# Kernel optimization log

Measured on AMD Instinct MI355X. Metric: run time of the kernel, lower is better.

## Reference

```python
import jax, jax.numpy as jnp
import numpy as np

N = 768
C = 256  # in_features == out_features (required by Linear(in_features+3, 1))

def _leaky(x):
    return jnp.where(x >= 0, x, 0.2 * x)

def setup_inputs() -> dict:
    key = jax.random.key(0)
    ks = jax.random.split(key, 10)
    features = jax.random.normal(ks[0], (N, C), dtype=jnp.float32)
    coordinates = jax.random.normal(ks[1], (N, 3), dtype=jnp.float32)
    adj = jax.random.uniform(ks[2], (N, N), dtype=jnp.float32)  # unused by forward, kept for signature fidelity
    # Learned params
    FC = jax.random.normal(ks[3], (C, C), dtype=jnp.float32) * (1.414 / jnp.sqrt(C))
    # Conv1d(2,1,kernel=1): weight [out=1, in=2, k=1] -> 2 scalars + bias
    fc_w = jax.random.normal(ks[4], (2,), dtype=jnp.float32) * 0.5
    fc_b = jax.random.normal(ks[5], (1,), dtype=jnp.float32) * 0.1
    sc_w = jax.random.normal(ks[6], (2,), dtype=jnp.float32) * 0.5
    sc_b = jax.random.normal(ks[7], (1,), dtype=jnp.float32) * 0.1
    # Linear(C+3, 1)
    lin_w = jax.random.normal(ks[8], (C + 3,), dtype=jnp.float32) * (1.0 / jnp.sqrt(C + 3))
    lin_b = jax.random.normal(ks[9], (1,), dtype=jnp.float32) * 0.1
    return {"features": features, "coordinates": coordinates, "adj": adj,
            "FC": FC, "fc_w": fc_w, "fc_b": fc_b, "sc_w": sc_w, "sc_b": sc_b,
            "lin_w": lin_w, "lin_b": lin_b}

def reference(features, coordinates, adj, FC, fc_w, fc_b, sc_w, sc_b, lin_w, lin_b):
    n = features.shape[0]
    f_input = features @ FC  # [N, C]
    # torch's repeat(1,N).view + repeat(N,1) builds pairs (i, j); the 1x1 Conv1d over
    # the 2 stacked channels is exactly w0*x_i + w1*x_j + b, then LeakyReLU(0.2).
    f_map = _leaky(fc_w[0] * f_input[:, None, :] + fc_w[1] * f_input[None, :, :] + fc_b[0])  # [N,N,C]
    s_map = _leaky(sc_w[0] * coordinates[:, None, :] + sc_w[1] * coordinates[None, :, :] + sc_b[0])  # [N,N,3]
    # Linear(C+3, 1) on cat([f_map, s_map], -1), then LeakyReLU -> [N, N]
    scores = _leaky(jnp.einsum('ijc,c->ij', f_map, lin_w[:f_input.shape[1]])
                    + jnp.einsum('ijk,k->ij', s_map, lin_w[f_input.shape[1]:])
                    + lin_b[0])
    attention = jax.nn.softmax(scores, axis=1)  # row softmax (dim=1)
    h_prime = attention @ f_input  # [N, C]
    return jax.nn.elu(h_prime)  # concat=True path
```

## Files before the change

kernel.cpp:

```cpp
#include <hip/hip_runtime.h>
#include <math.h>

#define NN 768
#define CC 256
#define TI 3
#define JC 256
#define NJC 3

__device__ __forceinline__ float leaky(float x) { return x >= 0.0f ? x : 0.2f * x; }

__device__ __forceinline__ float waveMax(float v) {
    #pragma unroll
    for (int o = 32; o > 0; o >>= 1) v = fmaxf(v, __shfl_xor(v, o, 64));
    return v;
}
__device__ __forceinline__ float waveSum(float v) {
    #pragma unroll
    for (int o = 32; o > 0; o >>= 1) v += __shfl_xor(v, o, 64);
    return v;
}

__global__ __launch_bounds__(768) void k_prep(
    const float* __restrict__ features,
    const float* __restrict__ FC,
    const float* __restrict__ fc_w,
    const float* __restrict__ fc_b,
    const float* __restrict__ lin_w,
    float* __restrict__ f,
    float* __restrict__ g,
    float* __restrict__ D0,
    float* __restrict__ D1,
    float4* __restrict__ ut4)
{
    __shared__ float sA[TI * CC];
    __shared__ float sF[TI * CC];
    __shared__ float sredD[12], sredW[12];

    const int t  = threadIdx.x;
    const int r  = t >> 8;
    const int c  = t & 255;
    const int i0 = blockIdx.x * TI;

    sA[r * CC + c] = features[(i0 + r) * CC + c];
    __syncthreads();

    float a = 0.f;
    const float* fcp = FC + c;
    const float* ap  = sA + r * CC;
    #pragma unroll 8
    for (int k = 0; k < CC; ++k)
        a = fmaf(ap[k], fcp[k * CC], a);

    const float w1 = fc_w[1], b = fc_b[0];
    f[(i0 + r) * CC + c] = a;
    g[c * NN + i0 + r]   = fmaf(w1, a, b);
    sF[r * CC + c] = a;

    const float lw = lin_w[c];
    float dv = waveSum(lw * a);
    float wv = waveSum(lw);
    const int wid = t >> 6;
    if ((t & 63) == 0) { sredD[wid] = dv; sredW[wid] = wv; }
    __syncthreads();
    if (t < TI) {
        float D = sredD[t*4] + sredD[t*4+1] + sredD[t*4+2] + sredD[t*4+3];
        float W = sredW[t*4] + sredW[t*4+1] + sredW[t*4+2] + sredW[t*4+3];
        D0[i0 + t] = fc_w[0] * D;
        D1[i0 + t] = fmaf(w1, D, b * W);
    }
    if (t < CC) {
        const float w0 = fc_w[0];
        ut4[blockIdx.x * CC + t] = make_float4(w0 * sF[t],
                                               w0 * sF[CC + t],
                                               w0 * sF[2*CC + t],
                                               0.4f * lin_w[t]);
    }
}

__global__ __launch_bounds__(256) void k_attn(
    const float* __restrict__ f,
    const float* __restrict__ g,
    const float4* __restrict__ ut4,
    const float* __restrict__ D0,
    const float* __restrict__ D1,
    const float* __restrict__ coords,
    const float* __restrict__ sc_w,
    const float* __restrict__ sc_b,
    const float* __restrict__ lin_w,
    const float* __restrict__ lin_b,
    float* __restrict__ hp,
    float* __restrict__ Mp,
    float* __restrict__ Lp)
{
    __shared__ float4 su4[CC];
    __shared__ float  spart[4][TI][JC];
    __shared__ float4 pp[JC];
    __shared__ float  hpart[4][TI][CC];
    __shared__ float4 sredm4[4];
    __shared__ float4 sreds4[4];

    const int t    = threadIdx.x;
    const int it   = blockIdx.x & 255;
    const int jc   = blockIdx.x >> 8;
    const int i0   = it * TI;
    const int jb   = jc * JC;
    const int j    = jb + t;
    const int w    = t >> 6;
    const int lane = t & 63;

    su4[t] = ut4[(size_t)it * CC + t];
    __syncthreads();

    float4 a0 = make_float4(0.f,0.f,0.f,0.f);
    float4 a1 = a0, a2 = a0;
    const float4* gq = (const float4*)g + (size_t)(w << 6) * (NN/4) + (jb >> 2) + lane;
    const float4* su = su4 + (w << 6);
    #pragma unroll 8
    for (int cc = 0; cc < 64; ++cc) {
        float4 gv = gq[cc * (NN/4)];
        float4 u  = su[cc];
        a0.x = fmaf(u.w, fabsf(u.x + gv.x), a0.x);
        a0.y = fmaf(u.w, fabsf(u.x + gv.y), a0.y);
        a0.z = fmaf(u.w, fabsf(u.x + gv.z), a0.z);
        a0.w = fmaf(u.w, fabsf(u.x + gv.w), a0.w);
        a1.x = fmaf(u.w, fabsf(u.y + gv.x), a1.x);
        a1.y = fmaf(u.w, fabsf(u.y + gv.y), a1.y);
        a1.z = fmaf(u.w, fabsf(u.y + gv.z), a1.z);
        a1.w = fmaf(u.w, fabsf(u.y + gv.w), a1.w);
        a2.x = fmaf(u.w, fabsf(u.z + gv.x), a2.x);
        a2.y = fmaf(u.w, fabsf(u.z + gv.y), a2.y);
        a2.z = fmaf(u.w, fabsf(u.z + gv.z), a2.z);
        a2.w = fmaf(u.w, fabsf(u.z + gv.w), a2.w);
    }
    *(float4*)&spart[w][0][4*lane] = a0;
    *(float4*)&spart[w][1][4*lane] = a1;
    *(float4*)&spart[w][2][4*lane] = a2;
    __syncthreads();

    float accs[3];
    #pragma unroll
    for (int rr = 0; rr < TI; ++rr)
        accs[rr] = spart[0][rr][t] + spart[1][rr][t]
                 + spart[2][rr][t] + spart[3][rr][t];

    const float sw0 = sc_w[0], sw1 = sc_w[1], sb = sc_b[0], lb = lin_b[0];
    const float lw30 = lin_w[CC], lw31 = lin_w[CC+1], lw32 = lin_w[CC+2];
    const float cj0 = fmaf(sw1, coords[j*3+0], sb);
    const float cj1 = fmaf(sw1, coords[j*3+1], sb);
    const float cj2 = fmaf(sw1, coords[j*3+2], sb);
    const float d1  = D1[j];
    float scv[3];
    #pragma unroll
    for (int rr = 0; rr < TI; ++rr) {
        const int i = i0 + rr;
        float sd = lw30 * leaky(fmaf(sw0, coords[i*3+0], cj0))
                 + lw31 * leaky(fmaf(sw0, coords[i*3+1], cj1))
                 + lw32 * leaky(fmaf(sw0, coords[i*3+2], cj2));
        scv[rr] = leaky(accs[rr] + sd + 0.6f * (D0[i] + d1) + lb);
    }

    {
        float v0 = waveMax(scv[0]);
        float v1 = waveMax(scv[1]);
        float v2 = waveMax(scv[2]);
        if (lane == 0) sredm4[w] = make_float4(v0, v1, v2, 0.f);
    }
    __syncthreads();
    float m[TI];
    {
        float4 x0 = sredm4[0], x1 = sredm4[1], x2 = sredm4[2], x3 = sredm4[3];
        m[0] = fmaxf(fmaxf(x0.x, x1.x), fmaxf(x2.x, x3.x));
        m[1] = fmaxf(fmaxf(x0.y, x1.y), fmaxf(x2.y, x3.y));
        m[2] = fmaxf(fmaxf(x0.z, x1.z), fmaxf(x2.z, x3.z));
    }
    float e0 = __expf(scv[0] - m[0]);
    float e1 = __expf(scv[1] - m[1]);
    float e2 = __expf(scv[2] - m[2]);
    pp[t] = make_float4(e0, e1, e2, 0.f);
    {
        float v0 = waveSum(e0);
        float v1 = waveSum(e1);
        float v2 = waveSum(e2);
        if (lane == 0) sreds4[w] = make_float4(v0, v1, v2, 0.f);
    }
    __syncthreads();
    if (t < TI) {
        float4 s0 = sreds4[0], s1 = sreds4[1], s2 = sreds4[2], s3 = sreds4[3];
        float l = (t == 0) ? (s0.x + s1.x + s2.x + s3.x)
                : (t == 1) ? (s0.y + s1.y + s2.y + s3.y)
                           : (s0.z + s1.z + s2.z + s3.z);
        float mm = (t == 0) ? m[0] : (t == 1) ? m[1] : m[2];
        Mp[(i0 + t) * NJC + jc] = mm;
        Lp[(i0 + t) * NJC + jc] = l;
    }

    float4 h0 = make_float4(0.f,0.f,0.f,0.f);
    float4 h1 = h0, h2 = h0;
    const float4* f4 = (const float4*)f;
    const int jsl = w * 64;
    #pragma unroll 4
    for (int jx = 0; jx < 64; ++jx) {
        const int jl = jsl + jx;
        float4 fv = f4[(size_t)(jb + jl) * 64 + lane];
        float4 e  = pp[jl];
        h0.x = fmaf(e.x, fv.x, h0.x); h0.y = fmaf(e.x, fv.y, h0.y);
        h0.z = fmaf(e.x, fv.z, h0.z); h0.w = fmaf(e.x, fv.w, h0.w);
        h1.x = fmaf(e.y, fv.x, h1.x); h1.y = fmaf(e.y, fv.y, h1.y);
        h1.z = fmaf(e.y, fv.z, h1.z); h1.w = fmaf(e.y, fv.w, h1.w);
        h2.x = fmaf(e.z, fv.x, h2.x); h2.y = fmaf(e.z, fv.y, h2.y);
        h2.z = fmaf(e.z, fv.z, h2.z); h2.w = fmaf(e.z, fv.w, h2.w);
    }
    *(float4*)&hpart[w][0][4*lane] = h0;
    *(float4*)&hpart[w][1][4*lane] = h1;
    *(float4*)&hpart[w][2][4*lane] = h2;
    __syncthreads();

    #pragma unroll
    for (int r = 0; r < TI; ++r) {
        float h = hpart[0][r][t] + hpart[1][r][t] + hpart[2][r][t] + hpart[3][r][t];
        hp[((size_t)jc * NN + i0 + r) * CC + t] = h;
    }
}

__global__ __launch_bounds__(256) void k_comb(
    const float* __restrict__ hp,
    const float* __restrict__ Mp,
    const float* __restrict__ Lp,
    float* __restrict__ out)
{
    const int t = threadIdx.x;
    const int i = blockIdx.x;

    float m0 = Mp[i*NJC+0], m1 = Mp[i*NJC+1], m2 = Mp[i*NJC+2];
    float M  = fmaxf(fmaxf(m0, m1), m2);
    float w0 = __expf(m0 - M), w1 = __expf(m1 - M), w2 = __expf(m2 - M);
    float den = w0*Lp[i*NJC+0] + w1*Lp[i*NJC+1] + w2*Lp[i*NJC+2];
    float inv = 1.0f / den;

    float num = w0 * hp[((size_t)0*NN + i)*CC + t]
              + w1 * hp[((size_t)1*NN + i)*CC + t]
              + w2 * hp[((size_t)2*NN + i)*CC + t];
    float v = num * inv;
    out[i*CC + t] = (v > 0.f) ? v : (__expf(v) - 1.0f);
}

extern "C" void kernel_launch(void* const* d_in, const int* in_sizes, int n_in,
                              void* d_out, int out_size, void* d_ws, size_t ws_size,
                              hipStream_t stream) {
    const float* features = (const float*)d_in[0];
    const float* coords   = (const float*)d_in[1];
    const float* FC       = (const float*)d_in[3];
    const float* fc_w     = (const float*)d_in[4];
    const float* fc_b     = (const float*)d_in[5];
    const float* sc_w     = (const float*)d_in[6];
    const float* sc_b     = (const float*)d_in[7];
    const float* lin_w    = (const float*)d_in[8];
    const float* lin_b    = (const float*)d_in[9];
    float* out = (float*)d_out;

    float* f  = (float*)d_ws;
    float* g  = f  + NN*CC;
    float* D0 = g  + CC*NN;
    float* D1 = D0 + NN;
    float* Mp = D1 + NN;
    float* Lp = Mp + NN*NJC;
    float* hp = Lp + NN*NJC;
    float4* ut4;
    {
        size_t off = (size_t)((char*)(hp + (size_t)NJC*NN*CC) - (char*)d_ws);
        off = (off + 15) & ~(size_t)15;
        ut4 = (float4*)((char*)d_ws + off);
    }

    k_prep<<<NN/TI, 768, 0, stream>>>(features, FC, fc_w, fc_b, lin_w, f, g, D0, D1, ut4);
    k_attn<<<(NN/TI)*NJC, 256, 0, stream>>>(f, g, ut4, D0, D1, coords, sc_w, sc_b,
                                            lin_w, lin_b, hp, Mp, Lp);
    k_comb<<<NN, 256, 0, stream>>>(hp, Mp, Lp, out);
}
```

Before: 111.5 us.

## Fuse split-j attention and combine kernel into one full-row kernel

Each block now handles all 768 columns for its three rows with 768 threads, so the softmax max and sum are computed exactly in-block. This removes the partial-result workspace (hp, Mp, Lp) and the separate combine kernel launch. The cost is fewer, larger blocks (256 blocks of 768 threads) with larger shared-memory usage, which may reduce latency hiding.

```diff
diff --git a/kernel.cpp b/kernel.cpp
--- a/kernel.cpp
+++ b/kernel.cpp
@@ -5,7 +5,6 @@
 #define CC 256
 #define TI 3
 #define JC 256
-#define NJC 3
 
 __device__ __forceinline__ float leaky(float x) { return x >= 0.0f ? x : 0.2f * x; }
 
@@ -77,7 +76,7 @@
     }
 }
 
-__global__ __launch_bounds__(256) void k_attn(
+__global__ __launch_bounds__(768) void k_attn2(
     const float* __restrict__ f,
     const float* __restrict__ g,
     const float4* __restrict__ ut4,
@@ -88,33 +87,31 @@
     const float* __restrict__ sc_b,
     const float* __restrict__ lin_w,
     const float* __restrict__ lin_b,
-    float* __restrict__ hp,
-    float* __restrict__ Mp,
-    float* __restrict__ Lp)
+    float* __restrict__ out)
 {
     __shared__ float4 su4[CC];
-    __shared__ float  spart[4][TI][JC];
-    __shared__ float4 pp[JC];
-    __shared__ float  hpart[4][TI][CC];
-    __shared__ float4 sredm4[4];
-    __shared__ float4 sreds4[4];
+    __shared__ float  sbig[4 * TI * NN];
+    __shared__ float4 pp[NN];
+    __shared__ float4 sredm4[12];
+    __shared__ float4 sreds4[12];
 
     const int t    = threadIdx.x;
-    const int it   = blockIdx.x & 255;
-    const int jc   = blockIdx.x >> 8;
+    const int it   = blockIdx.x;
     const int i0   = it * TI;
-    const int jb   = jc * JC;
-    const int j    = jb + t;
     const int w    = t >> 6;
     const int lane = t & 63;
 
-    su4[t] = ut4[(size_t)it * CC + t];
-    __syncthreads();
+    if (t < CC) su4[t] = ut4[(size_t)it * CC + t];
+    __syncthreads();
+
+    const int cs = w & 3;
+    const int js = w >> 2;
+    const int jb = js * JC;
 
     float4 a0 = make_float4(0.f,0.f,0.f,0.f);
     float4 a1 = a0, a2 = a0;
-    const float4* gq = (const float4*)g + (size_t)(w << 6) * (NN/4) + (jb >> 2) + lane;
-    const float4* su = su4 + (w << 6);
+    const float4* gq = (const float4*)g + (size_t)(cs << 6) * (NN/4) + (jb >> 2) + lane;
+    const float4* su = su4 + (cs << 6);
     #pragma unroll 8
     for (int cc = 0; cc < 64; ++cc) {
         float4 gv = gq[cc * (NN/4)];
@@ -132,16 +129,17 @@
         a2.z = fmaf(u.w, fabsf(u.z + gv.z), a2.z);
         a2.w = fmaf(u.w, fabsf(u.z + gv.w), a2.w);
     }
-    *(float4*)&spart[w][0][4*lane] = a0;
-    *(float4*)&spart[w][1][4*lane] = a1;
-    *(float4*)&spart[w][2][4*lane] = a2;
-    __syncthreads();
-
-    float accs[3];
+    *(float4*)&sbig[(cs*TI + 0)*NN + jb + 4*lane] = a0;
+    *(float4*)&sbig[(cs*TI + 1)*NN + jb + 4*lane] = a1;
+    *(float4*)&sbig[(cs*TI + 2)*NN + jb + 4*lane] = a2;
+    __syncthreads();
+
+    const int j = t;
+    float accs[TI];
     #pragma unroll
     for (int rr = 0; rr < TI; ++rr)
-        accs[rr] = spart[0][rr][t] + spart[1][rr][t]
-                 + spart[2][rr][t] + spart[3][rr][t];
+        accs[rr] = sbig[(0*TI + rr)*NN + j] + sbig[(1*TI + rr)*NN + j]
+                 + sbig[(2*TI + rr)*NN + j] + sbig[(3*TI + rr)*NN + j];
 
     const float sw0 = sc_w[0], sw1 = sc_w[1], sb = sc_b[0], lb = lin_b[0];
     const float lw30 = lin_w[CC], lw31 = lin_w[CC+1], lw32 = lin_w[CC+2];
@@ -149,7 +147,7 @@
     const float cj1 = fmaf(sw1, coords[j*3+1], sb);
     const float cj2 = fmaf(sw1, coords[j*3+2], sb);
     const float d1  = D1[j];
-    float scv[3];
+    float scv[TI];
     #pragma unroll
     for (int rr = 0; rr < TI; ++rr) {
         const int i = i0 + rr;
@@ -166,16 +164,15 @@
         if (lane == 0) sredm4[w] = make_float4(v0, v1, v2, 0.f);
     }
     __syncthreads();
-    float m[TI];
-    {
-        float4 x0 = sredm4[0], x1 = sredm4[1], x2 = sredm4[2], x3 = sredm4[3];
-        m[0] = fmaxf(fmaxf(x0.x, x1.x), fmaxf(x2.x, x3.x));
-        m[1] = fmaxf(fmaxf(x0.y, x1.y), fmaxf(x2.y, x3.y));
-        m[2] = fmaxf(fmaxf(x0.z, x1.z), fmaxf(x2.z, x3.z));
-    }
-    float e0 = __expf(scv[0] - m[0]);
-    float e1 = __expf(scv[1] - m[1]);
-    float e2 = __expf(scv[2] - m[2]);
+    float m0 = -1e30f, m1 = -1e30f, m2 = -1e30f;
+    #pragma unroll
+    for (int k = 0; k < 12; ++k) {
+        float4 x = sredm4[k];
+        m0 = fmaxf(m0, x.x); m1 = fmaxf(m1, x.y); m2 = fmaxf(m2, x.z);
+    }
+    float e0 = __expf(scv[0] - m0);
+    float e1 = __expf(scv[1] - m1);
+    float e2 = __expf(scv[2] - m2);
     pp[t] = make_float4(e0, e1, e2, 0.f);
     {
         float v0 = waveSum(e0);
@@ -184,15 +181,13 @@
         if (lane == 0) sreds4[w] = make_float4(v0, v1, v2, 0.f);
     }
     __syncthreads();
-    if (t < TI) {
-        float4 s0 = sreds4[0], s1 = sreds4[1], s2 = sreds4[2], s3 = sreds4[3];
-        float l = (t == 0) ? (s0.x + s1.x + s2.x + s3.x)
-                : (t == 1) ? (s0.y + s1.y + s2.y + s3.y)
-                           : (s0.z + s1.z + s2.z + s3.z);
-        float mm = (t == 0) ? m[0] : (t == 1) ? m[1] : m[2];
-        Mp[(i0 + t) * NJC + jc] = mm;
-        Lp[(i0 + t) * NJC + jc] = l;
-    }
+    float l0 = 0.f, l1 = 0.f, l2 = 0.f;
+    #pragma unroll
+    for (int k = 0; k < 12; ++k) {
+        float4 x = sreds4[k];
+        l0 += x.x; l1 += x.y; l2 += x.z;
+    }
+    const float inv0 = 1.f / l0, inv1 = 1.f / l1, inv2 = 1.f / l2;
 
     float4 h0 = make_float4(0.f,0.f,0.f,0.f);
     float4 h1 = h0, h2 = h0;
@@ -201,7 +196,7 @@
     #pragma unroll 4
     for (int jx = 0; jx < 64; ++jx) {
         const int jl = jsl + jx;
-        float4 fv = f4[(size_t)(jb + jl) * 64 + lane];
+        float4 fv = f4[(size_t)jl * 64 + lane];
         float4 e  = pp[jl];
         h0.x = fmaf(e.x, fv.x, h0.x); h0.y = fmaf(e.x, fv.y, h0.y);
         h0.z = fmaf(e.x, fv.z, h0.z); h0.w = fmaf(e.x, fv.w, h0.w);
@@ -210,38 +205,19 @@
         h2.x = fmaf(e.z, fv.x, h2.x); h2.y = fmaf(e.z, fv.y, h2.y);
         h2.z = fmaf(e.z, fv.z, h2.z); h2.w = fmaf(e.z, fv.w, h2.w);
     }
-    *(float4*)&hpart[w][0][4*lane] = h0;
-    *(float4*)&hpart[w][1][4*lane] = h1;
-    *(float4*)&hpart[w][2][4*lane] = h2;
-    __syncthreads();
-
-    #pragma unroll
-    for (int r = 0; r < TI; ++r) {
-        float h = hpart[0][r][t] + hpart[1][r][t] + hpart[2][r][t] + hpart[3][r][t];
-        hp[((size_t)jc * NN + i0 + r) * CC + t] = h;
-    }
-}
-
-__global__ __launch_bounds__(256) void k_comb(
-    const float* __restrict__ hp,
-    const float* __restrict__ Mp,
-    const float* __restrict__ Lp,
-    float* __restrict__ out)
-{
-    const int t = threadIdx.x;
-    const int i = blockIdx.x;
-
-    float m0 = Mp[i*NJC+0], m1 = Mp[i*NJC+1], m2 = Mp[i*NJC+2];
-    float M  = fmaxf(fmaxf(m0, m1), m2);
-    float w0 = __expf(m0 - M), w1 = __expf(m1 - M), w2 = __expf(m2 - M);
-    float den = w0*Lp[i*NJC+0] + w1*Lp[i*NJC+1] + w2*Lp[i*NJC+2];
-    float inv = 1.0f / den;
-
-    float num = w0 * hp[((size_t)0*NN + i)*CC + t]
-              + w1 * hp[((size_t)1*NN + i)*CC + t]
-              + w2 * hp[((size_t)2*NN + i)*CC + t];
-    float v = num * inv;
-    out[i*CC + t] = (v > 0.f) ? v : (__expf(v) - 1.0f);
+    *(float4*)&sbig[(w*TI + 0)*CC + 4*lane] = h0;
+    *(float4*)&sbig[(w*TI + 1)*CC + 4*lane] = h1;
+    *(float4*)&sbig[(w*TI + 2)*CC + 4*lane] = h2;
+    __syncthreads();
+
+    const int rr = t >> 8;
+    const int c  = t & 255;
+    float h = 0.f;
+    #pragma unroll
+    for (int k = 0; k < 12; ++k) h += sbig[(k*TI + rr)*CC + c];
+    const float inv = (rr == 0) ? inv0 : (rr == 1) ? inv1 : inv2;
+    float v = h * inv;
+    out[(i0 + rr)*CC + c] = (v > 0.f) ? v : (__expf(v) - 1.0f);
 }
 
 extern "C" void kernel_launch(void* const* d_in, const int* in_sizes, int n_in,
@@ -258,22 +234,13 @@
     const float* lin_b    = (const float*)d_in[9];
     float* out = (float*)d_out;
 
-    float* f  = (float*)d_ws;
+    float4* ut4 = (float4*)d_ws;
+    float* f  = (float*)(ut4 + (NN/TI)*CC);
     float* g  = f  + NN*CC;
     float* D0 = g  + CC*NN;
     float* D1 = D0 + NN;
-    float* Mp = D1 + NN;
-    float* Lp = Mp + NN*NJC;
-    float* hp = Lp + NN*NJC;
-    float4* ut4;
-    {
-        size_t off = (size_t)((char*)(hp + (size_t)NJC*NN*CC) - (char*)d_ws);
-        off = (off + 15) & ~(size_t)15;
-        ut4 = (float4*)((char*)d_ws + off);
-    }
 
     k_prep<<<NN/TI, 768, 0, stream>>>(features, FC, fc_w, fc_b, lin_w, f, g, D0, D1, ut4);
-    k_attn<<<(NN/TI)*NJC, 256, 0, stream>>>(f, g, ut4, D0, D1, coords, sc_w, sc_b,
-                                            lin_w, lin_b, hp, Mp, Lp);
-    k_comb<<<NN, 256, 0, stream>>>(hp, Mp, Lp, out);
-}
+    k_attn2<<<NN/TI, 768, 0, stream>>>(f, g, ut4, D0, D1, coords, sc_w, sc_b,
+                                       lin_w, lin_b, out);
+}
```

Result: no change. 110.6 us (-0.9%).
